# Performance work log

Measured on AMD Instinct MI355X. Metric: run time of the kernel, lower is better.

The kernel has to match this reference:

```python
import jax, jax.numpy as jnp
import numpy as np
from jax import lax

B, T, I, H, O = 64, 512, 256, 1024, 1


def setup_inputs() -> dict:
    key = jax.random.key(0)
    ks = jax.random.split(key, 7)
    s_ih = 1.0 / np.sqrt(H)
    return {
        "x": jax.random.normal(ks[0], (B, T, I), dtype=jnp.float32),
        "W_ih": jax.random.uniform(ks[1], (4 * H, I), minval=-s_ih, maxval=s_ih, dtype=jnp.float32),
        "W_hh": jax.random.uniform(ks[2], (4 * H, H), minval=-s_ih, maxval=s_ih, dtype=jnp.float32),
        "b_ih": jax.random.uniform(ks[3], (4 * H,), minval=-s_ih, maxval=s_ih, dtype=jnp.float32),
        "b_hh": jax.random.uniform(ks[4], (4 * H,), minval=-s_ih, maxval=s_ih, dtype=jnp.float32),
        "fc_W": jax.random.uniform(ks[5], (O, H), minval=-s_ih, maxval=s_ih, dtype=jnp.float32),
        "fc_b": jax.random.uniform(ks[6], (O,), minval=-s_ih, maxval=s_ih, dtype=jnp.float32),
    }


def reference(x, W_ih, W_hh, b_ih, b_hh, fc_W, fc_b):
    Bd, Td, _ = x.shape
    Hd = W_hh.shape[1]
    # Precompute input projections for all timesteps: [T, B, 4H]
    x_proj = jnp.einsum('bti,gi->tbg', x, W_ih) + b_ih + b_hh

    def step(carry, xt):
        h, c = carry
        gates = xt + h @ W_hh.T  # [B, 4H]
        i_g, f_g, g_g, o_g = jnp.split(gates, 4, axis=-1)  # PyTorch order i,f,g,o
        i_g = jax.nn.sigmoid(i_g)
        f_g = jax.nn.sigmoid(f_g)
        g_g = jnp.tanh(g_g)
        o_g = jax.nn.sigmoid(o_g)
        c_new = f_g * c + i_g * g_g
        h_new = o_g * jnp.tanh(c_new)
        return (h_new, c_new), None

    h0 = jnp.zeros((Bd, Hd), dtype=x.dtype)
    c0 = jnp.zeros((Bd, Hd), dtype=x.dtype)
    (h_last, _), _ = lax.scan(step, (h0, c0), x_proj)
    out = jnp.tanh(h_last)          # tanh on last hidden state
    return out @ fc_W.T + fc_b      # [B, O]
```

## Files before the change

kernel.cpp:

```cpp
#include <hip/hip_runtime.h>
#include <hip/hip_bf16.h>


typedef __bf16 bf16_t;
typedef bf16_t b16x8 __attribute__((ext_vector_type(8)));
typedef float  f32x4 __attribute__((ext_vector_type(4)));

#define TQ 512
#define IQ 256
#define HQ 1024

union U8 { b16x8 b; unsigned long long q[2]; unsigned short u[8]; };

__device__ __forceinline__ float bf2f(unsigned short s) {
    return __uint_as_float(((unsigned)s) << 16);
}
__device__ __forceinline__ unsigned short f2bf(float f) {
    unsigned u = __float_as_uint(f);
    u += 0x7fff + ((u >> 16) & 1);
    return (unsigned short)(u >> 16);
}
__device__ __forceinline__ b16x8 cvt84(float4 a, float4 b) {
    U8 r;
    r.u[0] = f2bf(a.x); r.u[1] = f2bf(a.y); r.u[2] = f2bf(a.z); r.u[3] = f2bf(a.w);
    r.u[4] = f2bf(b.x); r.u[5] = f2bf(b.y); r.u[6] = f2bf(b.z); r.u[7] = f2bf(b.w);
    return r.b;
}
__device__ __forceinline__ b16x8 load_h16(const unsigned short* p) {
    U8 r;
    r.q[0] = __hip_atomic_load((const unsigned long long*)p,
                               __ATOMIC_RELAXED, __HIP_MEMORY_SCOPE_AGENT);
    r.q[1] = __hip_atomic_load((const unsigned long long*)(p + 4),
                               __ATOMIC_RELAXED, __HIP_MEMORY_SCOPE_AGENT);
    return r.b;
}
__device__ __forceinline__ float sigm(float x) {
    return 1.f / (1.f + __expf(-x));
}
__device__ __forceinline__ float tanh_f(float v) {
    float x = fminf(fmaxf(v, -15.f), 15.f);
    float e = __expf(2.f * x);
    return (e - 1.f) / (e + 1.f);
}

__launch_bounds__(512, 2)
__global__ void lstm_persist(const float* __restrict__ x,
                             const float* __restrict__ Wih,
                             const float* __restrict__ Whh,
                             const float* __restrict__ bih,
                             const float* __restrict__ bhh,
                             const float* __restrict__ fcW,
                             const float* __restrict__ fcb,
                             float* __restrict__ out,
                             unsigned short* __restrict__ hbuf,
                             unsigned int* __restrict__ bar)
{
    __shared__ float red[2 * 8192];

    const int tid  = threadIdx.x;
    const int w    = tid >> 6;
    const int lane = tid & 63;
    const int bid  = blockIdx.x;
    const int bg   = bid & 3;
    const int ug   = bid >> 2;

    const int l16  = lane & 15;
    const int quad = lane >> 4;

    b16x8 wih[4];
    b16x8 whh[4][4];
    {
        const int koff = quad * 8;
        #pragma unroll
        for (int g = 0; g < 4; ++g) {
            int row = g * HQ + ug * 16 + l16;
            const float* p = Wih + (size_t)row * IQ + w * 32 + koff;
            float4 a = *(const float4*)p;
            float4 b = *(const float4*)(p + 4);
            wih[g] = cvt84(a, b);
            #pragma unroll
            for (int j = 0; j < 4; ++j) {
                int k0 = (w * 4 + j) * 32 + koff;
                const float* q = Whh + (size_t)row * HQ + k0;
                float4 c = *(const float4*)q;
                float4 d = *(const float4*)(q + 4);
                whh[j][g] = cvt84(c, d);
            }
        }
    }

    float c_st[4] = {0.f, 0.f, 0.f, 0.f};
    float bias_r[4];
    if (w == 0) {
        #pragma unroll
        for (int g = 0; g < 4; ++g) {
            int gr = g * HQ + ug * 16 + l16;
            bias_r[g] = bih[gr] + bhh[gr];
        }
    }

    unsigned int* fl = bar + (size_t)bg * 1024;
    const unsigned int* myfl = fl + (size_t)(w * 8 + (lane & 7)) * 16;

    const float* xbase = x + ((size_t)(bg * 16 + l16) * TQ) * IQ + w * 32 + quad * 8;
    float4 xa = *(const float4*)(xbase);
    float4 xb = *(const float4*)(xbase + 4);

    for (int t = 0; t < TQ; ++t) {
        const int p = t & 1;

        b16x8 ax = cvt84(xa, xb);
        f32x4 acc[4];
        #pragma unroll
        for (int g = 0; g < 4; ++g) {
            f32x4 z = {0.f, 0.f, 0.f, 0.f};
            acc[g] = __builtin_amdgcn_mfma_f32_16x16x32_bf16(ax, wih[g], z, 0, 0, 0);
        }

        if (t) {
            unsigned tv = (unsigned)t;
            unsigned v = __hip_atomic_load(myfl, __ATOMIC_RELAXED,
                                           __HIP_MEMORY_SCOPE_AGENT);
            while (!__all(v >= tv))
                v = __hip_atomic_load(myfl, __ATOMIC_RELAXED,
                                      __HIP_MEMORY_SCOPE_AGENT);
        }

        const unsigned short* hread = hbuf + ((size_t)p * 4 + bg) * (16 * HQ);
        b16x8 ah[4];
        #pragma unroll
        for (int j = 0; j < 4; ++j)
            ah[j] = load_h16(hread + (size_t)l16 * HQ + (w * 4 + j) * 32 + quad * 8);
        #pragma unroll
        for (int j = 0; j < 4; ++j) {
            #pragma unroll
            for (int g = 0; g < 4; ++g)
                acc[g] = __builtin_amdgcn_mfma_f32_16x16x32_bf16(ah[j], whh[j][g], acc[g], 0, 0, 0);
        }

        float* rb = &red[p * 8192];
        #pragma unroll
        for (int g = 0; g < 4; ++g)
            *(f32x4*)&rb[((w * 4 + g) * 64 + lane) * 4] = acc[g];
        __syncthreads();

        if (w == 0) {
            f32x4 gv[4];
            #pragma unroll
            for (int g = 0; g < 4; ++g) {
                f32x4 s = *(const f32x4*)&rb[((0 * 4 + g) * 64 + lane) * 4];
                #pragma unroll
                for (int ww = 1; ww < 8; ++ww)
                    s += *(const f32x4*)&rb[((ww * 4 + g) * 64 + lane) * 4];
                gv[g] = s;
            }
            unsigned short* hw = hbuf + ((size_t)(p ^ 1) * 4 + bg) * (16 * HQ)
                               + (size_t)ug * 16 + l16;
            #pragma unroll
            for (int r = 0; r < 4; ++r) {
                float gi = gv[0][r] + bias_r[0];
                float gf = gv[1][r] + bias_r[1];
                float gg = gv[2][r] + bias_r[2];
                float go = gv[3][r] + bias_r[3];
                float i_s = sigm(gi);
                float f_s = sigm(gf);
                float g_t = tanh_f(gg);
                float o_s = sigm(go);
                float c = f_s * c_st[r] + i_s * g_t;
                c_st[r] = c;
                float h = o_s * tanh_f(c);
                int b = quad * 4 + r;
                __hip_atomic_store(hw + (size_t)b * HQ, f2bf(h),
                                   __ATOMIC_RELAXED, __HIP_MEMORY_SCOPE_AGENT);
            }
            asm volatile("s_waitcnt vmcnt(0)" ::: "memory");
            if (lane == 0)
                __hip_atomic_store(fl + (size_t)ug * 16, (unsigned)(t + 1),
                                   __ATOMIC_RELAXED, __HIP_MEMORY_SCOPE_AGENT);
            size_t nt = (t + 1 < TQ) ? (size_t)(t + 1) * IQ : (size_t)t * IQ;
            xa = *(const float4*)(xbase + nt);
            xb = *(const float4*)(xbase + nt + 4);
        } else {
            size_t nt = (t + 1 < TQ) ? (size_t)(t + 1) * IQ : (size_t)t * IQ;
            xa = *(const float4*)(xbase + nt);
            xb = *(const float4*)(xbase + nt + 4);
        }
    }

    if (bid < 4) {
        if (w == 0) {
            const unsigned int* pf = fl + (size_t)lane * 16;
            unsigned v = __hip_atomic_load(pf, __ATOMIC_RELAXED,
                                           __HIP_MEMORY_SCOPE_AGENT);
            while (!__all(v >= (unsigned)TQ))
                v = __hip_atomic_load(pf, __ATOMIC_RELAXED,
                                      __HIP_MEMORY_SCOPE_AGENT);
        }
        __syncthreads();
        const unsigned short* hl = hbuf + (size_t)bg * (16 * HQ);
        float fb = fcb[0];
        #pragma unroll
        for (int r = 0; r < 2; ++r) {
            int b = w * 2 + r;
            float s = 0.f;
            #pragma unroll
            for (int j = 0; j < 16; ++j) {
                int u = j * 64 + lane;
                unsigned short hv = __hip_atomic_load(hl + b * HQ + u,
                                                      __ATOMIC_RELAXED,
                                                      __HIP_MEMORY_SCOPE_AGENT);
                s += tanh_f(bf2f(hv)) * fcW[u];
            }
            #pragma unroll
            for (int off = 32; off > 0; off >>= 1)
                s += __shfl_down(s, off);
            if (lane == 0) out[bg * 16 + b] = s + fb;
        }
    }
}

extern "C" void kernel_launch(void* const* d_in, const int* in_sizes, int n_in,
                              void* d_out, int out_size, void* d_ws, size_t ws_size,
                              hipStream_t stream) {
    (void)in_sizes; (void)n_in; (void)out_size; (void)ws_size;
    const float* x   = (const float*)d_in[0];
    const float* Wih = (const float*)d_in[1];
    const float* Whh = (const float*)d_in[2];
    const float* bih = (const float*)d_in[3];
    const float* bhh = (const float*)d_in[4];
    const float* fcW = (const float*)d_in[5];
    const float* fcb = (const float*)d_in[6];
    float* out = (float*)d_out;

    unsigned short* hbuf = (unsigned short*)d_ws;
    unsigned int*   bar  = (unsigned int*)((char*)d_ws + 262144);

    hipMemsetAsync(d_ws, 0, 262144 + 16384, stream);

    void* args[] = { &x, &Wih, &Whh, &bih, &bhh, &fcW, &fcb, &out, &hbuf, &bar };
    hipLaunchCooperativeKernel(reinterpret_cast<void*>(lstm_persist),
                               dim3(256), dim3(512), args, 0, stream);
}
```

Before: 2.375 ms.

## Spread gate reduction and LSTM cell update across four waves with per-wave flags

The cross-wave reduction and the cell nonlinearities were done by wave 0 alone. They are now split: waves 0-3 each reduce one gate, and 256 threads each handle one (batch, unit) pair, each writing its own h value. Each of those 4 waves publishes its own progress flag, and consumers poll 4 flags per block, double-buffering the loads in the spin loop. This shortens the serial critical path of each timestep. The cost is an extra __syncthreads, more flag traffic, and LDS reduced to a single buffer.

```diff
diff --git a/kernel.cpp b/kernel.cpp
--- a/kernel.cpp
+++ b/kernel.cpp
@@ -33,6 +33,9 @@
     r.q[1] = __hip_atomic_load((const unsigned long long*)(p + 4),
                                __ATOMIC_RELAXED, __HIP_MEMORY_SCOPE_AGENT);
     return r.b;
+}
+__device__ __forceinline__ unsigned ld_flag(const unsigned int* p) {
+    return __hip_atomic_load(p, __ATOMIC_RELAXED, __HIP_MEMORY_SCOPE_AGENT);
 }
 __device__ __forceinline__ float sigm(float x) {
     return 1.f / (1.f + __expf(-x));
@@ -55,7 +58,8 @@
                              unsigned short* __restrict__ hbuf,
                              unsigned int* __restrict__ bar)
 {
-    __shared__ float red[2 * 8192];
+    __shared__ float red[8192];
+    __shared__ float gbuf[1024];
 
     const int tid  = threadIdx.x;
     const int w    = tid >> 6;
@@ -89,18 +93,20 @@
         }
     }
 
-    float c_st[4] = {0.f, 0.f, 0.f, 0.f};
-    float bias_r[4];
-    if (w == 0) {
+    float c_st = 0.f;
+    float bias_r[4] = {0.f, 0.f, 0.f, 0.f};
+    if (tid < 256) {
+        int u = tid & 15;
         #pragma unroll
         for (int g = 0; g < 4; ++g) {
-            int gr = g * HQ + ug * 16 + l16;
+            int gr = g * HQ + ug * 16 + u;
             bias_r[g] = bih[gr] + bhh[gr];
         }
     }
 
     unsigned int* fl = bar + (size_t)bg * 1024;
-    const unsigned int* myfl = fl + (size_t)(w * 8 + (lane & 7)) * 16;
+    const unsigned int* myfl =
+        fl + (size_t)(8 * w + ((lane & 31) >> 2)) * 16 + (lane & 3);
 
     const float* xbase = x + ((size_t)(bg * 16 + l16) * TQ) * IQ + w * 32 + quad * 8;
     float4 xa = *(const float4*)(xbase);
@@ -118,12 +124,15 @@
         }
 
         if (t) {
-            unsigned tv = (unsigned)t;
-            unsigned v = __hip_atomic_load(myfl, __ATOMIC_RELAXED,
-                                           __HIP_MEMORY_SCOPE_AGENT);
-            while (!__all(v >= tv))
-                v = __hip_atomic_load(myfl, __ATOMIC_RELAXED,
-                                      __HIP_MEMORY_SCOPE_AGENT);
+            int tv = t;
+            unsigned va = ld_flag(myfl);
+            unsigned vb = ld_flag(myfl);
+            for (;;) {
+                if (__all((int)va >= tv)) break;
+                va = ld_flag(myfl);
+                if (__all((int)vb >= tv)) break;
+                vb = ld_flag(myfl);
+            }
         }
 
         const unsigned short* hread = hbuf + ((size_t)p * 4 + bg) * (16 * HQ);
@@ -138,63 +147,59 @@
                 acc[g] = __builtin_amdgcn_mfma_f32_16x16x32_bf16(ah[j], whh[j][g], acc[g], 0, 0, 0);
         }
 
-        float* rb = &red[p * 8192];
         #pragma unroll
         for (int g = 0; g < 4; ++g)
-            *(f32x4*)&rb[((w * 4 + g) * 64 + lane) * 4] = acc[g];
+            *(f32x4*)&red[((w * 4 + g) * 64 + lane) * 4] = acc[g];
         __syncthreads();
 
-        if (w == 0) {
-            f32x4 gv[4];
-            #pragma unroll
-            for (int g = 0; g < 4; ++g) {
-                f32x4 s = *(const f32x4*)&rb[((0 * 4 + g) * 64 + lane) * 4];
-                #pragma unroll
-                for (int ww = 1; ww < 8; ++ww)
-                    s += *(const f32x4*)&rb[((ww * 4 + g) * 64 + lane) * 4];
-                gv[g] = s;
-            }
-            unsigned short* hw = hbuf + ((size_t)(p ^ 1) * 4 + bg) * (16 * HQ)
-                               + (size_t)ug * 16 + l16;
-            #pragma unroll
-            for (int r = 0; r < 4; ++r) {
-                float gi = gv[0][r] + bias_r[0];
-                float gf = gv[1][r] + bias_r[1];
-                float gg = gv[2][r] + bias_r[2];
-                float go = gv[3][r] + bias_r[3];
-                float i_s = sigm(gi);
-                float f_s = sigm(gf);
-                float g_t = tanh_f(gg);
-                float o_s = sigm(go);
-                float c = f_s * c_st[r] + i_s * g_t;
-                c_st[r] = c;
-                float h = o_s * tanh_f(c);
-                int b = quad * 4 + r;
-                __hip_atomic_store(hw + (size_t)b * HQ, f2bf(h),
-                                   __ATOMIC_RELAXED, __HIP_MEMORY_SCOPE_AGENT);
-            }
-            asm volatile("s_waitcnt vmcnt(0)" ::: "memory");
-            if (lane == 0)
-                __hip_atomic_store(fl + (size_t)ug * 16, (unsigned)(t + 1),
-                                   __ATOMIC_RELAXED, __HIP_MEMORY_SCOPE_AGENT);
-            size_t nt = (t + 1 < TQ) ? (size_t)(t + 1) * IQ : (size_t)t * IQ;
-            xa = *(const float4*)(xbase + nt);
-            xb = *(const float4*)(xbase + nt + 4);
+        if (w < 4) {
+            f32x4 s = *(const f32x4*)&red[((0 * 4 + w) * 64 + lane) * 4];
+            #pragma unroll
+            for (int ww = 1; ww < 8; ++ww)
+                s += *(const f32x4*)&red[((ww * 4 + w) * 64 + lane) * 4];
+            #pragma unroll
+            for (int r = 0; r < 4; ++r)
+                gbuf[w * 256 + quad * 64 + r * 16 + l16] = s[r];
         } else {
             size_t nt = (t + 1 < TQ) ? (size_t)(t + 1) * IQ : (size_t)t * IQ;
             xa = *(const float4*)(xbase + nt);
             xb = *(const float4*)(xbase + nt + 4);
         }
+        __syncthreads();
+
+        if (tid < 256) {
+            int b = tid >> 4, u = tid & 15;
+            float gi = gbuf[0 * 256 + tid] + bias_r[0];
+            float gf = gbuf[1 * 256 + tid] + bias_r[1];
+            float gg = gbuf[2 * 256 + tid] + bias_r[2];
+            float go = gbuf[3 * 256 + tid] + bias_r[3];
+            float i_s = sigm(gi);
+            float f_s = sigm(gf);
+            float g_t = tanh_f(gg);
+            float o_s = sigm(go);
+            float c = f_s * c_st + i_s * g_t;
+            c_st = c;
+            float h = o_s * tanh_f(c);
+            unsigned short* hw = hbuf + ((size_t)(p ^ 1) * 4 + bg) * (16 * HQ)
+                               + (size_t)b * HQ + ug * 16 + u;
+            __hip_atomic_store(hw, f2bf(h),
+                               __ATOMIC_RELAXED, __HIP_MEMORY_SCOPE_AGENT);
+            asm volatile("s_waitcnt vmcnt(0)" ::: "memory");
+            if (lane == 0)
+                __hip_atomic_store(fl + (size_t)ug * 16 + w, (unsigned)(t + 1),
+                                   __ATOMIC_RELAXED, __HIP_MEMORY_SCOPE_AGENT);
+            asm volatile("" ::: "memory");
+            size_t nt = (t + 1 < TQ) ? (size_t)(t + 1) * IQ : (size_t)t * IQ;
+            xa = *(const float4*)(xbase + nt);
+            xb = *(const float4*)(xbase + nt + 4);
+        }
     }
 
     if (bid < 4) {
-        if (w == 0) {
-            const unsigned int* pf = fl + (size_t)lane * 16;
-            unsigned v = __hip_atomic_load(pf, __ATOMIC_RELAXED,
-                                           __HIP_MEMORY_SCOPE_AGENT);
-            while (!__all(v >= (unsigned)TQ))
-                v = __hip_atomic_load(pf, __ATOMIC_RELAXED,
-                                      __HIP_MEMORY_SCOPE_AGENT);
+        {
+            unsigned va = ld_flag(myfl);
+            while (!__all((int)va >= TQ))
+                va = ld_flag(myfl);
         }
         __syncthreads();
         const unsigned short* hl = hbuf + (size_t)bg * (16 * HQ);
```

Measured after the change: 2.589 ms. 9.0% more time.

## Replace per-step flag barrier with timestep-tagged hidden-state words

Applied to the files above, without the earlier changes.

Each hidden value is now stored as a 32-bit word that packs the bf16 value with the timestep tag. Consumers spin on the data itself until every loaded word carries the expected tag. This removes the separate flag store, the vmcnt(0) wait before it, and the flag polling round-trip from every recurrent step. In exchange the h buffer doubles in size and the loads become wider, and a full stale reload repeats on every spin, with s_sleep backoff after a few tries.

```diff
diff --git a/kernel.cpp b/kernel.cpp
--- a/kernel.cpp
+++ b/kernel.cpp
@@ -10,7 +10,7 @@
 #define IQ 256
 #define HQ 1024
 
-union U8 { b16x8 b; unsigned long long q[2]; unsigned short u[8]; };
+union U8 { b16x8 b; unsigned short u[8]; };
 
 __device__ __forceinline__ float bf2f(unsigned short s) {
     return __uint_as_float(((unsigned)s) << 16);
@@ -26,13 +26,12 @@
     r.u[4] = f2bf(b.x); r.u[5] = f2bf(b.y); r.u[6] = f2bf(b.z); r.u[7] = f2bf(b.w);
     return r.b;
 }
-__device__ __forceinline__ b16x8 load_h16(const unsigned short* p) {
-    U8 r;
-    r.q[0] = __hip_atomic_load((const unsigned long long*)p,
-                               __ATOMIC_RELAXED, __HIP_MEMORY_SCOPE_AGENT);
-    r.q[1] = __hip_atomic_load((const unsigned long long*)(p + 4),
-                               __ATOMIC_RELAXED, __HIP_MEMORY_SCOPE_AGENT);
-    return r.b;
+__device__ __forceinline__ unsigned long long ld8(const unsigned* p) {
+    return __hip_atomic_load((const unsigned long long*)p,
+                             __ATOMIC_RELAXED, __HIP_MEMORY_SCOPE_AGENT);
+}
+__device__ __forceinline__ unsigned ld4(const unsigned* p) {
+    return __hip_atomic_load(p, __ATOMIC_RELAXED, __HIP_MEMORY_SCOPE_AGENT);
 }
 __device__ __forceinline__ float sigm(float x) {
     return 1.f / (1.f + __expf(-x));
@@ -52,8 +51,7 @@
                              const float* __restrict__ fcW,
                              const float* __restrict__ fcb,
                              float* __restrict__ out,
-                             unsigned short* __restrict__ hbuf,
-                             unsigned int* __restrict__ bar)
+                             unsigned* __restrict__ hbuf)
 {
     __shared__ float red[2 * 8192];
 
@@ -99,8 +97,7 @@
         }
     }
 
-    unsigned int* fl = bar + (size_t)bg * 1024;
-    const unsigned int* myfl = fl + (size_t)(w * 8 + (lane & 7)) * 16;
+    const int ubase = w * 128 + quad * 8;
 
     const float* xbase = x + ((size_t)(bg * 16 + l16) * TQ) * IQ + w * 32 + quad * 8;
     float4 xa = *(const float4*)(xbase);
@@ -117,20 +114,42 @@
             acc[g] = __builtin_amdgcn_mfma_f32_16x16x32_bf16(ax, wih[g], z, 0, 0, 0);
         }
 
-        if (t) {
-            unsigned tv = (unsigned)t;
-            unsigned v = __hip_atomic_load(myfl, __ATOMIC_RELAXED,
-                                           __HIP_MEMORY_SCOPE_AGENT);
-            while (!__all(v >= tv))
-                v = __hip_atomic_load(myfl, __ATOMIC_RELAXED,
-                                      __HIP_MEMORY_SCOPE_AGENT);
-        }
-
-        const unsigned short* hread = hbuf + ((size_t)p * 4 + bg) * (16 * HQ);
+        const unsigned* hrow = hbuf + (((size_t)p * 4 + bg) * 16 + l16) * HQ;
+        unsigned long long v[16];
+        {
+            const unsigned tt = (unsigned)t;
+            int spins = 0;
+            for (;;) {
+                #pragma unroll
+                for (int j = 0; j < 4; ++j) {
+                    const unsigned* pj = hrow + ubase + j * 32;
+                    #pragma unroll
+                    for (int k = 0; k < 4; ++k)
+                        v[j * 4 + k] = ld8(pj + k * 2);
+                }
+                bool ok = true;
+                #pragma unroll
+                for (int i = 0; i < 16; ++i) {
+                    ok = ok && (((unsigned)(v[i] >> 16) & 0xffffu) == tt)
+                            && (((unsigned)(v[i] >> 48)) == tt);
+                }
+                if (__all(ok)) break;
+                if (++spins > 4) __builtin_amdgcn_s_sleep(1);
+            }
+        }
+
         b16x8 ah[4];
         #pragma unroll
-        for (int j = 0; j < 4; ++j)
-            ah[j] = load_h16(hread + (size_t)l16 * HQ + (w * 4 + j) * 32 + quad * 8);
+        for (int j = 0; j < 4; ++j) {
+            U8 tmp;
+            #pragma unroll
+            for (int k = 0; k < 4; ++k) {
+                unsigned long long q = v[j * 4 + k];
+                tmp.u[2 * k]     = (unsigned short)(q & 0xffffu);
+                tmp.u[2 * k + 1] = (unsigned short)((q >> 32) & 0xffffu);
+            }
+            ah[j] = tmp.b;
+        }
         #pragma unroll
         for (int j = 0; j < 4; ++j) {
             #pragma unroll
@@ -154,8 +173,9 @@
                     s += *(const f32x4*)&rb[((ww * 4 + g) * 64 + lane) * 4];
                 gv[g] = s;
             }
-            unsigned short* hw = hbuf + ((size_t)(p ^ 1) * 4 + bg) * (16 * HQ)
-                               + (size_t)ug * 16 + l16;
+            unsigned* hw = hbuf + ((size_t)(p ^ 1) * 4 + bg) * (16 * HQ)
+                         + (size_t)ug * 16 + l16;
+            const unsigned tagv = ((unsigned)(t + 1)) << 16;
             #pragma unroll
             for (int r = 0; r < 4; ++r) {
                 float gi = gv[0][r] + bias_r[0];
@@ -170,34 +190,20 @@
                 c_st[r] = c;
                 float h = o_s * tanh_f(c);
                 int b = quad * 4 + r;
-                __hip_atomic_store(hw + (size_t)b * HQ, f2bf(h),
+                __hip_atomic_store(hw + (size_t)b * HQ, tagv | (unsigned)f2bf(h),
                                    __ATOMIC_RELAXED, __HIP_MEMORY_SCOPE_AGENT);
             }
-            asm volatile("s_waitcnt vmcnt(0)" ::: "memory");
-            if (lane == 0)
-                __hip_atomic_store(fl + (size_t)ug * 16, (unsigned)(t + 1),
-                                   __ATOMIC_RELAXED, __HIP_MEMORY_SCOPE_AGENT);
+        }
+        {
             size_t nt = (t + 1 < TQ) ? (size_t)(t + 1) * IQ : (size_t)t * IQ;
             xa = *(const float4*)(xbase + nt);
             xb = *(const float4*)(xbase + nt + 4);
-        } else {
-            size_t nt = (t + 1 < TQ) ? (size_t)(t + 1) * IQ : (size_t)t * IQ;
-            xa = *(const float4*)(xbase + nt);
-            xb = *(const float4*)(xbase + nt + 4);
         }
     }
 
     if (bid < 4) {
-        if (w == 0) {
-            const unsigned int* pf = fl + (size_t)lane * 16;
-            unsigned v = __hip_atomic_load(pf, __ATOMIC_RELAXED,
-                                           __HIP_MEMORY_SCOPE_AGENT);
-            while (!__all(v >= (unsigned)TQ))
-                v = __hip_atomic_load(pf, __ATOMIC_RELAXED,
-                                      __HIP_MEMORY_SCOPE_AGENT);
-        }
-        __syncthreads();
-        const unsigned short* hl = hbuf + (size_t)bg * (16 * HQ);
+        const unsigned* hl = hbuf + (size_t)bg * (16 * HQ);
+        const unsigned ft = (unsigned)TQ;
         float fb = fcb[0];
         #pragma unroll
         for (int r = 0; r < 2; ++r) {
@@ -206,10 +212,9 @@
             #pragma unroll
             for (int j = 0; j < 16; ++j) {
                 int u = j * 64 + lane;
-                unsigned short hv = __hip_atomic_load(hl + b * HQ + u,
-                                                      __ATOMIC_RELAXED,
-                                                      __HIP_MEMORY_SCOPE_AGENT);
-                s += tanh_f(bf2f(hv)) * fcW[u];
+                unsigned hv = ld4(hl + (size_t)b * HQ + u);
+                while ((hv >> 16) != ft) hv = ld4(hl + (size_t)b * HQ + u);
+                s += tanh_f(bf2f((unsigned short)(hv & 0xffffu))) * fcW[u];
             }
             #pragma unroll
             for (int off = 32; off > 0; off >>= 1)
@@ -232,12 +237,11 @@
     const float* fcb = (const float*)d_in[6];
     float* out = (float*)d_out;
 
-    unsigned short* hbuf = (unsigned short*)d_ws;
-    unsigned int*   bar  = (unsigned int*)((char*)d_ws + 262144);
-
-    hipMemsetAsync(d_ws, 0, 262144 + 16384, stream);
-
-    void* args[] = { &x, &Wih, &Whh, &bih, &bhh, &fcW, &fcb, &out, &hbuf, &bar };
+    unsigned* hbuf = (unsigned*)d_ws;
+
+    hipMemsetAsync(d_ws, 0, 524288, stream);
+
+    void* args[] = { &x, &Wih, &Whh, &bih, &bhh, &fcW, &fcb, &out, &hbuf };
     hipLaunchCooperativeKernel(reinterpret_cast<void*>(lstm_persist),
                                dim3(256), dim3(512), args, 0, stream);
 }
```

After: 8.623 ms. +263.1%, slower.

## Split per-step flag wait into per-chunk waits overlapped with h loads

Applied to the files above, without the earlier changes.

The single wait on all eight producer flags before loading h is replaced by four narrower waits, one per 32-unit chunk of h. Each wait checks only the two producer flags that own that chunk, so each chunk can be loaded as soon as its producers finish rather than after every producer does. The spin loop alternates two outstanding flag loads to keep polling latency down. The final barrier is also changed so every wave polls the flags instead of only wave 0, and this adds more flag traffic and spin instructions in exchange for finer-grained dependency tracking.

```diff
diff --git a/kernel.cpp b/kernel.cpp
--- a/kernel.cpp
+++ b/kernel.cpp
@@ -33,6 +33,9 @@
     r.q[1] = __hip_atomic_load((const unsigned long long*)(p + 4),
                                __ATOMIC_RELAXED, __HIP_MEMORY_SCOPE_AGENT);
     return r.b;
+}
+__device__ __forceinline__ unsigned ld_flag(const unsigned int* p) {
+    return __hip_atomic_load(p, __ATOMIC_RELAXED, __HIP_MEMORY_SCOPE_AGENT);
 }
 __device__ __forceinline__ float sigm(float x) {
     return 1.f / (1.f + __expf(-x));
@@ -100,6 +103,10 @@
     }
 
     unsigned int* fl = bar + (size_t)bg * 1024;
+    const unsigned int* flj[4];
+    #pragma unroll
+    for (int j = 0; j < 4; ++j)
+        flj[j] = fl + (size_t)((w * 4 + j) * 2 + (lane & 1)) * 16;
     const unsigned int* myfl = fl + (size_t)(w * 8 + (lane & 7)) * 16;
 
     const float* xbase = x + ((size_t)(bg * 16 + l16) * TQ) * IQ + w * 32 + quad * 8;
@@ -117,20 +124,23 @@
             acc[g] = __builtin_amdgcn_mfma_f32_16x16x32_bf16(ax, wih[g], z, 0, 0, 0);
         }
 
-        if (t) {
-            unsigned tv = (unsigned)t;
-            unsigned v = __hip_atomic_load(myfl, __ATOMIC_RELAXED,
-                                           __HIP_MEMORY_SCOPE_AGENT);
-            while (!__all(v >= tv))
-                v = __hip_atomic_load(myfl, __ATOMIC_RELAXED,
-                                      __HIP_MEMORY_SCOPE_AGENT);
-        }
-
         const unsigned short* hread = hbuf + ((size_t)p * 4 + bg) * (16 * HQ);
         b16x8 ah[4];
         #pragma unroll
-        for (int j = 0; j < 4; ++j)
+        for (int j = 0; j < 4; ++j) {
+            if (t) {
+                unsigned va = ld_flag(flj[j]);
+                unsigned vb = ld_flag(flj[j]);
+                for (;;) {
+                    if (__all((int)va >= t)) break;
+                    va = ld_flag(flj[j]);
+                    if (__all((int)vb >= t)) break;
+                    vb = ld_flag(flj[j]);
+                }
+            }
             ah[j] = load_h16(hread + (size_t)l16 * HQ + (w * 4 + j) * 32 + quad * 8);
+        }
+
         #pragma unroll
         for (int j = 0; j < 4; ++j) {
             #pragma unroll
@@ -177,6 +187,7 @@
             if (lane == 0)
                 __hip_atomic_store(fl + (size_t)ug * 16, (unsigned)(t + 1),
                                    __ATOMIC_RELAXED, __HIP_MEMORY_SCOPE_AGENT);
+            asm volatile("" ::: "memory");
             size_t nt = (t + 1 < TQ) ? (size_t)(t + 1) * IQ : (size_t)t * IQ;
             xa = *(const float4*)(xbase + nt);
             xb = *(const float4*)(xbase + nt + 4);
@@ -188,13 +199,10 @@
     }
 
     if (bid < 4) {
-        if (w == 0) {
-            const unsigned int* pf = fl + (size_t)lane * 16;
-            unsigned v = __hip_atomic_load(pf, __ATOMIC_RELAXED,
-                                           __HIP_MEMORY_SCOPE_AGENT);
-            while (!__all(v >= (unsigned)TQ))
-                v = __hip_atomic_load(pf, __ATOMIC_RELAXED,
-                                      __HIP_MEMORY_SCOPE_AGENT);
+        {
+            unsigned va = ld_flag(myfl);
+            while (!__all((int)va >= TQ))
+                va = ld_flag(myfl);
         }
         __syncthreads();
         const unsigned short* hl = hbuf + (size_t)bg * (16 * HQ);
```

New measurement: 2.419 ms. No clear change (+1.8%).
